# Kernel optimization log

Measured on AMD Instinct MI355X. Metric: run time of the kernel, lower is better.

Reference implementation:

```python
import jax, jax.numpy as jnp
import numpy as np
from jax import lax

TIME_STEP = 5
VTH = 1.0
A = 1.0
TAU = 0.5
DROP_RATE = 0.1
BLOCK_SIZE = 7


@jax.custom_vjp
def spike(u):
    return (u > VTH).astype(u.dtype)

def _spike_fwd(u):
    return spike(u), u

def _spike_bwd(u, g):
    # surrogate: rectangular window of width `a` around Vth
    hu = (jnp.abs(u - VTH) < A / 2).astype(g.dtype) / A
    return (g * hu,)

spike.defvjp(_spike_fwd, _spike_bwd)


def _block_mask(mask_rand):
    # mask_rand: [T*bs, H, W] uniform(0,1)
    gamma = DROP_RATE / BLOCK_SIZE ** 2
    mask = (mask_rand < gamma).astype(jnp.float32)
    pad = BLOCK_SIZE // 2
    pooled = lax.reduce_window(
        mask, -jnp.inf, lax.max,
        window_dimensions=(1, BLOCK_SIZE, BLOCK_SIZE),
        window_strides=(1, 1, 1),
        padding=((0, 0), (pad, pad), (pad, pad)))
    return 1.0 - pooled  # [T*bs, H, W]


def setup_inputs() -> dict:
    key = jax.random.key(0)
    k1, k2 = jax.random.split(key)
    T, bs, C, H, W = TIME_STEP, 32, 64, 64, 64
    x = jax.random.normal(k1, (T * bs, C, H, W), dtype=jnp.float32)
    mask_rand = jax.random.uniform(k2, (T * bs, H, W), dtype=jnp.float32)
    return {"x": x, "mask_rand": mask_rand}


def reference(x, mask_rand):
    N, C, H, W = x.shape
    bs = N // TIME_STEP
    bm = _block_mask(mask_rand)                      # [T*bs, H, W]
    x_t = x.reshape(TIME_STEP, bs, C, H, W)
    bm_t = bm.reshape(TIME_STEP, bs, H, W)

    def step(u, inp):
        xt, bmt = inp
        u = TAU * u * (1.0 - spike(u)) + xt          # leaky integrate w/ reset
        s = spike(u)
        o = s * bmt[:, None, :, :]                   # dropblock mask per sample
        return u, o

    u0 = jnp.zeros((bs, C, H, W), dtype=x.dtype)
    _, o = lax.scan(step, u0, (x_t, bm_t))
    return o.reshape(N, C, H, W)
```

## Files before the change

kernel.cpp:

```cpp
#include <hip/hip_runtime.h>


#define TSTEPS 5
#define BSZ 32
#define CHN 64
#define HH 64
#define WW 64

typedef float v4f __attribute__((ext_vector_type(4)));

__global__ __launch_bounds__(256) void bm_kernel(const float* __restrict__ mr,
                                                 float* __restrict__ bm) {
    const float GAMMA = (float)(0.1 / 49.0);
    int wave = blockIdx.x * 4 + (threadIdx.x >> 6);
    int lane = threadIdx.x & 63;
    int h = wave & (HH - 1);
    int n = wave >> 6;

    const float* base = mr + (size_t)n * (HH * WW) + lane;
    bool drop = false;
#pragma unroll
    for (int dh = -3; dh <= 3; ++dh) {
        int hh = h + dh;
        if (hh >= 0 && hh < HH) drop = drop || (base[hh * WW] < GAMMA);
    }
    unsigned long long m = __ballot(drop);
    unsigned long long s = m | (m << 1) | (m << 2) | (m << 3)
                             | (m >> 1) | (m >> 2) | (m >> 3);
    bm[(size_t)wave * WW + lane] = ((s >> lane) & 1ull) ? 0.0f : 1.0f;
}

__global__ __launch_bounds__(256) void lif_kernel(const float* __restrict__ x,
                                                  const float* __restrict__ bm,
                                                  float* __restrict__ o) {
    const int HW4 = HH * WW / 4;
    int idx = blockIdx.x * blockDim.x + threadIdx.x;
    int hw4 = idx & (HW4 - 1);
    int c = (idx >> 10) & (CHN - 1);
    int b = idx >> 16;
    if (b >= BSZ) return;

    size_t xoff = (((size_t)b * CHN + c) * (size_t)(HH * WW)) + (size_t)hw4 * 4;
    size_t moff = ((size_t)b * (size_t)(HH * WW)) + (size_t)hw4 * 4;
    const size_t XT = (size_t)BSZ * CHN * HH * WW;
    const size_t MT = (size_t)BSZ * HH * WW;

    v4f u = {0.f, 0.f, 0.f, 0.f};
#pragma unroll
    for (int t = 0; t < TSTEPS; ++t) {
        v4f xv = __builtin_nontemporal_load((const v4f*)(x + xoff + (size_t)t * XT));
        v4f mv = *(const v4f*)(bm + moff + (size_t)t * MT);
        u.x = (u.x > 1.0f ? 0.0f : 0.5f * u.x) + xv.x;
        u.y = (u.y > 1.0f ? 0.0f : 0.5f * u.y) + xv.y;
        u.z = (u.z > 1.0f ? 0.0f : 0.5f * u.z) + xv.z;
        u.w = (u.w > 1.0f ? 0.0f : 0.5f * u.w) + xv.w;
        v4f ov;
        ov.x = (u.x > 1.0f) ? mv.x : 0.0f;
        ov.y = (u.y > 1.0f) ? mv.y : 0.0f;
        ov.z = (u.z > 1.0f) ? mv.z : 0.0f;
        ov.w = (u.w > 1.0f) ? mv.w : 0.0f;
        __builtin_nontemporal_store(ov, (v4f*)(o + xoff + (size_t)t * XT));
    }
}

extern "C" void kernel_launch(void* const* d_in, const int* in_sizes, int n_in,
                              void* d_out, int out_size, void* d_ws, size_t ws_size,
                              hipStream_t stream) {
    const float* x = (const float*)d_in[0];
    const float* mask_rand = (const float*)d_in[1];
    float* out = (float*)d_out;
    float* bm = (float*)d_ws;

    const int bm_rows = TSTEPS * BSZ * HH;
    const int lif_threads = BSZ * CHN * (HH * WW / 4);

    bm_kernel<<<bm_rows / 4, 256, 0, stream>>>(mask_rand, bm);
    lif_kernel<<<(lif_threads + 255) / 256, 256, 0, stream>>>(x, bm, out);
}
```

Measured before the change: 280.0 us.

## Fuse dropblock mask computation into LIF kernel using shared-memory bitmasks

The two kernels are merged into one. Each block computes the dropblock mask for two rows of one sample across all timesteps as 64-bit ballot bitmasks in shared memory, then runs the LIF recurrence over all channels for those rows. This removes the float mask round-trip through global memory and one kernel launch. In exchange there are only 1024 blocks, each looping over 8 channels serially, and a sync stall while the mask is built, which may reduce memory-level parallelism.

Measured after the change: 284.7 us. No clear change (+1.7%).

```diff
diff --git a/kernel.cpp b/kernel.cpp
--- a/kernel.cpp
+++ b/kernel.cpp
@@ -9,57 +9,64 @@
 
 typedef float v4f __attribute__((ext_vector_type(4)));
 
-__global__ __launch_bounds__(256) void bm_kernel(const float* __restrict__ mr,
-                                                 float* __restrict__ bm) {
+__global__ __launch_bounds__(256) void fused_kernel(const float* __restrict__ x,
+                                                    const float* __restrict__ mr,
+                                                    float* __restrict__ o) {
+    __shared__ unsigned long long bmbits[2 * TSTEPS];
     const float GAMMA = (float)(0.1 / 49.0);
-    int wave = blockIdx.x * 4 + (threadIdx.x >> 6);
-    int lane = threadIdx.x & 63;
-    int h = wave & (HH - 1);
-    int n = wave >> 6;
+    int b = blockIdx.x >> 5;
+    int g = blockIdx.x & 31;
+    int r0 = g << 1;
+    int tid = threadIdx.x;
+    int wave = tid >> 6;
+    int lane = tid & 63;
 
-    const float* base = mr + (size_t)n * (HH * WW) + lane;
-    bool drop = false;
+    for (int m = wave; m < 2 * TSTEPS; m += 4) {
+        int row = r0 + (m & 1);
+        int t = m >> 1;
+        const float* base = mr + (size_t)(t * BSZ + b) * (HH * WW) + lane;
+        bool drop = false;
 #pragma unroll
-    for (int dh = -3; dh <= 3; ++dh) {
-        int hh = h + dh;
-        if (hh >= 0 && hh < HH) drop = drop || (base[hh * WW] < GAMMA);
+        for (int dh = -3; dh <= 3; ++dh) {
+            int hh = row + dh;
+            if (hh >= 0 && hh < HH) drop = drop || (base[hh * WW] < GAMMA);
+        }
+        unsigned long long mm = __ballot(drop);
+        unsigned long long s = mm | (mm << 1) | (mm << 2) | (mm << 3)
+                                  | (mm >> 1) | (mm >> 2) | (mm >> 3);
+        if (lane == 0) bmbits[m] = s;
     }
-    unsigned long long m = __ballot(drop);
-    unsigned long long s = m | (m << 1) | (m << 2) | (m << 3)
-                             | (m >> 1) | (m >> 2) | (m >> 3);
-    bm[(size_t)wave * WW + lane] = ((s >> lane) & 1ull) ? 0.0f : 1.0f;
-}
+    __syncthreads();
 
-__global__ __launch_bounds__(256) void lif_kernel(const float* __restrict__ x,
-                                                  const float* __restrict__ bm,
-                                                  float* __restrict__ o) {
-    const int HW4 = HH * WW / 4;
-    int idx = blockIdx.x * blockDim.x + threadIdx.x;
-    int hw4 = idx & (HW4 - 1);
-    int c = (idx >> 10) & (CHN - 1);
-    int b = idx >> 16;
-    if (b >= BSZ) return;
+    int pos = tid & 31;
+    int row_in = pos >> 4;
+    int col4 = pos & 15;
+    unsigned int nib[TSTEPS];
+#pragma unroll
+    for (int t = 0; t < TSTEPS; ++t)
+        nib[t] = (unsigned int)((bmbits[t * 2 + row_in] >> (col4 * 4)) & 0xFull);
 
-    size_t xoff = (((size_t)b * CHN + c) * (size_t)(HH * WW)) + (size_t)hw4 * 4;
-    size_t moff = ((size_t)b * (size_t)(HH * WW)) + (size_t)hw4 * 4;
+    int c0 = tid >> 5;
     const size_t XT = (size_t)BSZ * CHN * HH * WW;
-    const size_t MT = (size_t)BSZ * HH * WW;
-
-    v4f u = {0.f, 0.f, 0.f, 0.f};
+    size_t base_off = (size_t)b * CHN * (HH * WW)
+                    + (size_t)(r0 + row_in) * WW + (size_t)col4 * 4;
+    for (int c = c0; c < CHN; c += 8) {
+        size_t xoff = base_off + (size_t)c * (HH * WW);
+        v4f u = {0.f, 0.f, 0.f, 0.f};
 #pragma unroll
-    for (int t = 0; t < TSTEPS; ++t) {
-        v4f xv = __builtin_nontemporal_load((const v4f*)(x + xoff + (size_t)t * XT));
-        v4f mv = *(const v4f*)(bm + moff + (size_t)t * MT);
-        u.x = (u.x > 1.0f ? 0.0f : 0.5f * u.x) + xv.x;
-        u.y = (u.y > 1.0f ? 0.0f : 0.5f * u.y) + xv.y;
-        u.z = (u.z > 1.0f ? 0.0f : 0.5f * u.z) + xv.z;
-        u.w = (u.w > 1.0f ? 0.0f : 0.5f * u.w) + xv.w;
-        v4f ov;
-        ov.x = (u.x > 1.0f) ? mv.x : 0.0f;
-        ov.y = (u.y > 1.0f) ? mv.y : 0.0f;
-        ov.z = (u.z > 1.0f) ? mv.z : 0.0f;
-        ov.w = (u.w > 1.0f) ? mv.w : 0.0f;
-        __builtin_nontemporal_store(ov, (v4f*)(o + xoff + (size_t)t * XT));
+        for (int t = 0; t < TSTEPS; ++t) {
+            v4f xv = __builtin_nontemporal_load((const v4f*)(x + xoff + (size_t)t * XT));
+            u.x = (u.x > 1.0f ? 0.0f : 0.5f * u.x) + xv.x;
+            u.y = (u.y > 1.0f ? 0.0f : 0.5f * u.y) + xv.y;
+            u.z = (u.z > 1.0f ? 0.0f : 0.5f * u.z) + xv.z;
+            u.w = (u.w > 1.0f ? 0.0f : 0.5f * u.w) + xv.w;
+            v4f ov;
+            ov.x = (u.x > 1.0f && !(nib[t] & 1u)) ? 1.0f : 0.0f;
+            ov.y = (u.y > 1.0f && !(nib[t] & 2u)) ? 1.0f : 0.0f;
+            ov.z = (u.z > 1.0f && !(nib[t] & 4u)) ? 1.0f : 0.0f;
+            ov.w = (u.w > 1.0f && !(nib[t] & 8u)) ? 1.0f : 0.0f;
+            __builtin_nontemporal_store(ov, (v4f*)(o + xoff + (size_t)t * XT));
+        }
     }
 }
 
@@ -69,11 +76,8 @@
     const float* x = (const float*)d_in[0];
     const float* mask_rand = (const float*)d_in[1];
     float* out = (float*)d_out;
-    float* bm = (float*)d_ws;
+    (void)d_ws; (void)ws_size;
 
-    const int bm_rows = TSTEPS * BSZ * HH;
-    const int lif_threads = BSZ * CHN * (HH * WW / 4);
-
-    bm_kernel<<<bm_rows / 4, 256, 0, stream>>>(mask_rand, bm);
-    lif_kernel<<<(lif_threads + 255) / 256, 256, 0, stream>>>(x, bm, out);
+    const int nblocks = BSZ * (HH / 2);
+    fused_kernel<<<nblocks, 256, 0, stream>>>(x, mask_rand, out);
 }
```

## Pack dropblock mask into per-row 64-bit bitmasks instead of floats

Applied to the files above, without the earlier changes.

The block-mask kernel now writes one 64-bit ballot word per image row instead of a float per pixel. The LIF kernel reads that word and tests four bits per thread to gate the spike output. This cuts the mask write and read traffic and makes the mask footprint tiny enough to stay in cache. The cost is a few extra bit operations and a scalar 64-bit load per timestep, which many lanes share.

Result: no change. 278.1 us (-0.7%).

```diff
diff --git a/kernel.cpp b/kernel.cpp
--- a/kernel.cpp
+++ b/kernel.cpp
@@ -9,13 +9,13 @@
 
 typedef float v4f __attribute__((ext_vector_type(4)));
 
-__global__ __launch_bounds__(256) void bm_kernel(const float* __restrict__ mr,
-                                                 float* __restrict__ bm) {
+__global__ __launch_bounds__(256) void bm_bits_kernel(const float* __restrict__ mr,
+                                                      unsigned long long* __restrict__ bmbits) {
     const float GAMMA = (float)(0.1 / 49.0);
-    int wave = blockIdx.x * 4 + (threadIdx.x >> 6);
+    int row = blockIdx.x * 4 + (threadIdx.x >> 6);
     int lane = threadIdx.x & 63;
-    int h = wave & (HH - 1);
-    int n = wave >> 6;
+    int h = row & (HH - 1);
+    int n = row >> 6;
 
     const float* base = mr + (size_t)n * (HH * WW) + lane;
     bool drop = false;
@@ -27,11 +27,11 @@
     unsigned long long m = __ballot(drop);
     unsigned long long s = m | (m << 1) | (m << 2) | (m << 3)
                              | (m >> 1) | (m >> 2) | (m >> 3);
-    bm[(size_t)wave * WW + lane] = ((s >> lane) & 1ull) ? 0.0f : 1.0f;
+    if (lane == 0) bmbits[row] = s;
 }
 
 __global__ __launch_bounds__(256) void lif_kernel(const float* __restrict__ x,
-                                                  const float* __restrict__ bm,
+                                                  const unsigned long long* __restrict__ bmbits,
                                                   float* __restrict__ o) {
     const int HW4 = HH * WW / 4;
     int idx = blockIdx.x * blockDim.x + threadIdx.x;
@@ -40,25 +40,29 @@
     int b = idx >> 16;
     if (b >= BSZ) return;
 
+    int h = hw4 >> 4;
+    int col4 = hw4 & 15;
+    int sh = col4 * 4;
+
     size_t xoff = (((size_t)b * CHN + c) * (size_t)(HH * WW)) + (size_t)hw4 * 4;
-    size_t moff = ((size_t)b * (size_t)(HH * WW)) + (size_t)hw4 * 4;
     const size_t XT = (size_t)BSZ * CHN * HH * WW;
-    const size_t MT = (size_t)BSZ * HH * WW;
+    int mrow = b * HH + h;
+    const int MT = BSZ * HH;
 
     v4f u = {0.f, 0.f, 0.f, 0.f};
 #pragma unroll
     for (int t = 0; t < TSTEPS; ++t) {
         v4f xv = __builtin_nontemporal_load((const v4f*)(x + xoff + (size_t)t * XT));
-        v4f mv = *(const v4f*)(bm + moff + (size_t)t * MT);
+        unsigned int nib = (unsigned int)((bmbits[mrow + t * MT] >> sh) & 0xFull);
         u.x = (u.x > 1.0f ? 0.0f : 0.5f * u.x) + xv.x;
         u.y = (u.y > 1.0f ? 0.0f : 0.5f * u.y) + xv.y;
         u.z = (u.z > 1.0f ? 0.0f : 0.5f * u.z) + xv.z;
         u.w = (u.w > 1.0f ? 0.0f : 0.5f * u.w) + xv.w;
         v4f ov;
-        ov.x = (u.x > 1.0f) ? mv.x : 0.0f;
-        ov.y = (u.y > 1.0f) ? mv.y : 0.0f;
-        ov.z = (u.z > 1.0f) ? mv.z : 0.0f;
-        ov.w = (u.w > 1.0f) ? mv.w : 0.0f;
+        ov.x = (u.x > 1.0f && !(nib & 1u)) ? 1.0f : 0.0f;
+        ov.y = (u.y > 1.0f && !(nib & 2u)) ? 1.0f : 0.0f;
+        ov.z = (u.z > 1.0f && !(nib & 4u)) ? 1.0f : 0.0f;
+        ov.w = (u.w > 1.0f && !(nib & 8u)) ? 1.0f : 0.0f;
         __builtin_nontemporal_store(ov, (v4f*)(o + xoff + (size_t)t * XT));
     }
 }
@@ -69,11 +73,11 @@
     const float* x = (const float*)d_in[0];
     const float* mask_rand = (const float*)d_in[1];
     float* out = (float*)d_out;
-    float* bm = (float*)d_ws;
+    unsigned long long* bmbits = (unsigned long long*)d_ws;
 
     const int bm_rows = TSTEPS * BSZ * HH;
     const int lif_threads = BSZ * CHN * (HH * WW / 4);
 
-    bm_kernel<<<bm_rows / 4, 256, 0, stream>>>(mask_rand, bm);
-    lif_kernel<<<(lif_threads + 255) / 256, 256, 0, stream>>>(x, bm, out);
+    bm_bits_kernel<<<bm_rows / 4, 256, 0, stream>>>(mask_rand, bmbits);
+    lif_kernel<<<(lif_threads + 255) / 256, 256, 0, stream>>>(x, bmbits, out);
 }
```
